# Performance work log

Hardware: AMD Instinct MI355X
Metric: run time of the kernel (lower is better)

## Reference

```python
import jax, jax.numpy as jnp
import numpy as np

B, S, DIM, H, HD = 2, 2048, 512, 8, 64
VD = DIM // H  # 64
QK = H * HD


def setup_inputs() -> dict:
    key = jax.random.key(0)
    k1, k2, k3, k4, k5 = jax.random.split(key, 5)
    x = jax.random.normal(k1, (B, S, DIM), dtype=jnp.float32)
    mask = jax.random.bernoulli(k2, 0.5, (B, S))
    # per-position rotation matrices, scaled to keep activations O(1)
    rotator = jax.random.normal(k3, (B, S, HD, HD), dtype=jnp.float32) / np.sqrt(HD)
    # torch Linear weights: [out_features, in_features], no bias
    W_trans = jax.random.normal(k4, (2 * QK + DIM, DIM), dtype=jnp.float32) / np.sqrt(DIM)
    W_o = jax.random.normal(k5, (DIM, DIM), dtype=jnp.float32) / np.sqrt(DIM)
    return {"x": x, "mask": mask, "rotator": rotator, "W_trans": W_trans, "W_o": W_o}


def _taylor_attention(qs, ks, vs, mask):
    # 2nd-order Taylor approximation of exp for softmax weights
    # qs/ks: [B,S,H,HD], vs: [B,S,H,VD], mask: [B,S] key mask
    scores = jnp.einsum('bqhd,bkhd->bhqk', qs, ks) / np.sqrt(HD)
    w = 1.0 + scores + 0.5 * scores * scores
    w = jnp.where(mask[:, None, None, :], w, 0.0)
    w = w / jnp.sum(w, axis=-1, keepdims=True)
    out = jnp.einsum('bhqk,bkhd->bqhd', w, vs)
    return out.reshape(out.shape[0], out.shape[1], -1)  # [B,S,DIM]


def reference(x, mask, rotator, W_trans, W_o):
    t = x @ W_trans.T  # [B,S,2*QK+DIM]
    qs = t[..., :QK].reshape(B, S, H, HD)
    ks = t[..., QK:2 * QK].reshape(B, S, H, HD)
    vs = t[..., 2 * QK:].reshape(B, S, H, VD)
    sel = mask[..., None, None]
    qs = jnp.where(sel, jnp.einsum('bsij,bshj->bshi', rotator, qs), qs)
    ks = jnp.where(sel, jnp.einsum('bsij,bshj->bshi', rotator, ks), ks)
    out = _taylor_attention(qs, ks, vs, mask)
    return out @ W_o.T
```

## Files before the change

### kernel.cpp

```cpp
#include <hip/hip_runtime.h>
#include <hip/hip_bf16.h>

#define B_    2
#define S_    2048
#define DIM_  512
#define H_    8
#define HD_   64
#define TOUT_ 1536
#define ROWS_ (B_ * S_)

typedef unsigned short ushort_t;
typedef __attribute__((ext_vector_type(8))) __bf16 bf16x8;
typedef __attribute__((ext_vector_type(4))) float floatx4;

#define AS_GLB __attribute__((address_space(1)))
#define AS_LDS __attribute__((address_space(3)))

__device__ __forceinline__ unsigned short f2bfu(float f) {
    unsigned u = __float_as_uint(f);
    unsigned r = (u + 0x7fffu + ((u >> 16) & 1u)) >> 16;
    return (unsigned short)r;
}
__device__ __forceinline__ bf16x8 cvt8(const float* p) {
    float4 a = *reinterpret_cast<const float4*>(p);
    float4 b = *reinterpret_cast<const float4*>(p + 4);
    ushort_t o[8] = {f2bfu(a.x), f2bfu(a.y), f2bfu(a.z), f2bfu(a.w),
                     f2bfu(b.x), f2bfu(b.y), f2bfu(b.z), f2bfu(b.w)};
    return *reinterpret_cast<bf16x8*>(o);
}

__global__ void tmha_mask(const unsigned char* mb, int* wm) {
    __shared__ int s_bf, s_f, s_u8;
    int tid = threadIdx.x;
    if (tid == 0) { s_bf = 0; s_f = 0; s_u8 = 0; }
    __syncthreads();
    int cbf = 0, cf = 0, cu8 = 0;
    for (int i = tid; i < 4096; i += 256) {
        unsigned char v = mb[i];
        if (v == 0x3F || v == 0x80) {
            cf++;
            if ((i & 3) == 1) cbf++;
        } else if (v != 0 && (i & 3) != 0) {
            cu8++;
        }
    }
    atomicAdd(&s_bf, cbf); atomicAdd(&s_f, cf); atomicAdd(&s_u8, cu8);
    __syncthreads();
    int cls = (s_bf > 0) ? 2 : (s_f > 0) ? 3 : (s_u8 > 0) ? 0 : 1;
    for (int i = tid; i < ROWS_; i += 256) {
        int v;
        if (cls == 0)      v = (mb[i] != 0);
        else if (cls == 1) v = (reinterpret_cast<const int*>(mb)[i] != 0);
        else if (cls == 2) v = ((reinterpret_cast<const unsigned short*>(mb)[i] & 0x7fffu) != 0);
        else               v = ((reinterpret_cast<const unsigned int*>(mb)[i] & 0x7fffffffu) != 0);
        wm[i] = v;
    }
}

#define XN4_  (ROWS_ * DIM_ / 4)
#define WTN4_ (TOUT_ * DIM_ / 4)
#define WON4_ (DIM_ * DIM_ / 4)
__global__ __launch_bounds__(256) void cast3_bf16(const float* __restrict__ x,
                                                  const float* __restrict__ wt,
                                                  const float* __restrict__ wo,
                                                  ushort_t* __restrict__ xb,
                                                  ushort_t* __restrict__ wtb,
                                                  ushort_t* __restrict__ wob) {
    int i = blockIdx.x * 256 + threadIdx.x;
    const float* s; ushort_t* d; int off;
    if (i < XN4_)              { s = x;  d = xb;  off = i; }
    else if (i < XN4_ + WTN4_) { s = wt; d = wtb; off = i - XN4_; }
    else                       { s = wo; d = wob; off = i - XN4_ - WTN4_; }
    float4 v = reinterpret_cast<const float4*>(s)[off];
    ushort_t o[4] = {f2bfu(v.x), f2bfu(v.y), f2bfu(v.z), f2bfu(v.w)};
    reinterpret_cast<uint2*>(d)[off] = *reinterpret_cast<uint2*>(o);
}

template <int TM, int N, int K, bool OUT_BF16>
__global__ __launch_bounds__(256) void mfma_gemm_bt(const ushort_t* __restrict__ A,
                                                    const ushort_t* __restrict__ Bm,
                                                    void* __restrict__ Cout) {
    constexpr int FM = (TM + 31) / 32;
    __shared__ __align__(16) ushort_t As[TM * 64];
    __shared__ __align__(16) ushort_t Bs[128 * 64];
    int tid = threadIdx.x;
    int lane = tid & 63;
    int wv = tid >> 6;
    int wm = wv >> 1, wn = wv & 1;
    int quad = lane >> 4;
    int mrow = lane & 15;
    int bx = blockIdx.x;
    int by = blockIdx.y;

    floatx4 acc[FM][4];
#pragma unroll
    for (int i = 0; i < FM; i++)
#pragma unroll
        for (int j = 0; j < 4; j++) acc[i][j] = (floatx4){0.f, 0.f, 0.f, 0.f};

    for (int k0 = 0; k0 < K; k0 += 64) {
#pragma unroll
        for (int t = 0; t < TM / 32; t++) {
            int p = (wv * (TM / 32) + t) * 64 + lane;
            int row = p >> 3, cp = p & 7;
            int gc = cp ^ (row & 7);
            const ushort_t* ga = A + (size_t)(by * TM + row) * K + k0 + gc * 8;
            __builtin_amdgcn_global_load_lds((const AS_GLB unsigned int*)ga,
                                             (AS_LDS unsigned int*)&As[(size_t)(wv * (TM / 32) + t) * 64 * 8],
                                             16, 0, 0);
        }
#pragma unroll
        for (int t = 0; t < 4; t++) {
            int p = (wv * 4 + t) * 64 + lane;
            int row = p >> 3, cp = p & 7;
            int gc = cp ^ (row & 7);
            const ushort_t* gb = Bm + (size_t)(bx * 128 + row) * K + k0 + gc * 8;
            __builtin_amdgcn_global_load_lds((const AS_GLB unsigned int*)gb,
                                             (AS_LDS unsigned int*)&Bs[(size_t)(wv * 4 + t) * 64 * 8],
                                             16, 0, 0);
        }
        __syncthreads();
#pragma unroll
        for (int ks = 0; ks < 64; ks += 32) {
            int c = (ks >> 3) + quad;
            bf16x8 af[FM], bf[4];
#pragma unroll
            for (int i = 0; i < FM; i++) {
                int row = wm * (TM / 2) + i * 16 + mrow;
                int pos = row * 8 + (c ^ (row & 7));
                af[i] = *reinterpret_cast<const bf16x8*>(&As[pos * 8]);
            }
#pragma unroll
            for (int j = 0; j < 4; j++) {
                int row = wn * 64 + j * 16 + mrow;
                int pos = row * 8 + (c ^ (row & 7));
                bf[j] = *reinterpret_cast<const bf16x8*>(&Bs[pos * 8]);
            }
#pragma unroll
            for (int i = 0; i < FM; i++)
#pragma unroll
                for (int j = 0; j < 4; j++)
                    acc[i][j] = __builtin_amdgcn_mfma_f32_16x16x32_bf16(af[i], bf[j], acc[i][j], 0, 0, 0);
        }
        __syncthreads();
    }

    int col0 = bx * 128 + wn * 64 + mrow;
    int row0 = by * TM + wm * (TM / 2) + quad * 4;
    if constexpr (OUT_BF16) {
        ushort_t* C = reinterpret_cast<ushort_t*>(Cout);
#pragma unroll
        for (int i = 0; i < FM; i++)
#pragma unroll
            for (int j = 0; j < 4; j++)
#pragma unroll
                for (int r = 0; r < 4; r++)
                    C[(size_t)(row0 + i * 16 + r) * N + col0 + j * 16] = f2bfu(acc[i][j][r]);
    } else {
        float* C = reinterpret_cast<float*>(Cout);
#pragma unroll
        for (int i = 0; i < FM; i++)
#pragma unroll
            for (int j = 0; j < 4; j++)
#pragma unroll
                for (int r = 0; r < 4; r++)
                    C[(size_t)(row0 + i * 16 + r) * N + col0 + j * 16] = acc[i][j][r];
    }
}

__global__ __launch_bounds__(256) void rot_qk_mfma(const ushort_t* __restrict__ t,
                                                   const float* __restrict__ rotG,
                                                   const int* __restrict__ wm,
                                                   ushort_t* __restrict__ Qb,
                                                   ushort_t* __restrict__ Kb) {
    int lane = threadIdx.x & 63;
    int wv = threadIdx.x >> 6;
    int row = blockIdx.x * 4 + wv;
    int b = row >> 11, s = row & 2047;
    int lm = lane & 15, quad = lane >> 4;
    const ushort_t* trow = t + (size_t)row * TOUT_;
    int kb = s >> 4, l = s & 15;

    if (wm[row]) {
        bf16x8 af[2];
#pragma unroll
        for (int kc = 0; kc < 2; kc++)
            af[kc] = *reinterpret_cast<const bf16x8*>(trow + lm * 64 + kc * 32 + quad * 8);

        const float* R = rotG + (size_t)row * 4096;
        floatx4 dacc[4];
#pragma unroll
        for (int nb = 0; nb < 4; nb++) dacc[nb] = (floatx4){0.f, 0.f, 0.f, 0.f};
#pragma unroll
        for (int nb = 0; nb < 4; nb++)
#pragma unroll
            for (int kc = 0; kc < 2; kc++) {
                bf16x8 bfr = cvt8(R + (size_t)(nb * 16 + lm) * 64 + kc * 32 + quad * 8);
                dacc[nb] = __builtin_amdgcn_mfma_f32_16x16x32_bf16(af[kc], bfr, dacc[nb], 0, 0, 0);
            }
#pragma unroll
        for (int nb = 0; nb < 4; nb++)
#pragma unroll
            for (int r = 0; r < 4; r++) {
                int vec = quad * 4 + r;
                int hh = vec & 7;
                ushort_t v = f2bfu(dacc[nb][r]);
                if (vec >= 8) {
                    int c = nb * 2 + (lm >> 3), e = lm & 7;
                    Kb[(((size_t)(b * 8 + hh) * 128 + kb) * 8 + c) * 128 + l * 8 + e] = v;
                } else {
                    Qb[((size_t)(b * 8 + hh) * 2048 + s) * 64 + nb * 16 + lm] = v;
                }
            }
    } else {
#pragma unroll
        for (int nb = 0; nb < 4; nb++)
#pragma unroll
            for (int r = 0; r < 4; r++) {
                int vec = quad * 4 + r;
                int hh = vec & 7;
                ushort_t v = trow[vec * 64 + nb * 16 + lm];
                if (vec >= 8) {
                    int c = nb * 2 + (lm >> 3), e = lm & 7;
                    Kb[(((size_t)(b * 8 + hh) * 128 + kb) * 8 + c) * 128 + l * 8 + e] = v;
                } else {
                    Qb[((size_t)(b * 8 + hh) * 2048 + s) * 64 + nb * 16 + lm] = v;
                }
            }
    }
}

__global__ __launch_bounds__(256) void prep_vt(const ushort_t* __restrict__ t,
                                               const int* __restrict__ wm,
                                               ushort_t* __restrict__ VtG) {
    __shared__ ushort_t tile[64][72];
    __shared__ float mrow[64];
    int st = blockIdx.x;
    int bh = blockIdx.y;
    int b = bh >> 3, h = bh & 7;
    int tid = threadIdx.x;
    if (tid < 64) mrow[tid] = wm[b * 2048 + st * 64 + tid] ? 1.0f : 0.0f;
#pragma unroll
    for (int i = 0; i < 2; i++) {
        int q = i * 256 + tid;
        int r = q >> 3, c8 = (q & 7) * 8;
        uint4 v = *reinterpret_cast<const uint4*>(
            t + (size_t)(b * 2048 + st * 64 + r) * TOUT_ + 1024 + h * 64 + c8);
        *reinterpret_cast<uint4*>(&tile[r][c8]) = v;
    }
    __syncthreads();
#pragma unroll
    for (int i = 0; i < 8; i++) {
        int e = i * 256 + tid;
        int d = e >> 5, sl = (e & 31) * 2;
        unsigned u0 = (mrow[sl]     != 0.f) ? (unsigned)tile[sl][d]     : 0u;
        unsigned u1 = (mrow[sl + 1] != 0.f) ? (unsigned)tile[sl + 1][d] : 0u;
        *reinterpret_cast<unsigned int*>(VtG + ((size_t)bh * 65 + d) * 2048 + st * 64 + sl) = u0 | (u1 << 16);
    }
    if (tid < 32) {
        int sl = tid * 2;
        unsigned m0 = mrow[sl]     != 0.f ? 0x3F80u : 0u;
        unsigned m1 = mrow[sl + 1] != 0.f ? 0x3F80u : 0u;
        *reinterpret_cast<unsigned int*>(VtG + ((size_t)bh * 65 + 64) * 2048 + st * 64 + sl) = m0 | (m1 << 16);
    }
}

__global__ __launch_bounds__(256) void tmha_attn_mfma(const ushort_t* __restrict__ Qb,
                                                      const ushort_t* __restrict__ KbF,
                                                      const ushort_t* __restrict__ VtG,
                                                      float* __restrict__ numer,
                                                      float* __restrict__ den) {
    __shared__ __align__(16) ushort_t Vs[2][520 * 8];
    __shared__ __align__(16) ushort_t Ps[512 * 8];
    int tid = threadIdx.x;
    int lane = tid & 63;
    int wv = tid >> 6;
    int lm = lane & 15;
    int quad = lane >> 4;
    int qt = blockIdx.x;
    int h = blockIdx.y;
    int z = blockIdx.z;
    int b = z >> 1;
    int ks = z & 1;
    int bh = b * 8 + h;

    const ushort_t* Kf  = KbF + (size_t)bh * 128 * 1024;
    const ushort_t* Vbh = VtG + (size_t)bh * 65 * 2048;

    bf16x8 qf[2];
    {
        const ushort_t* qp = Qb + ((size_t)bh * 2048 + qt * 64 + wv * 16 + lm) * 64 + quad * 8;
        qf[0] = *reinterpret_cast<const bf16x8*>(qp);
        qf[1] = *reinterpret_cast<const bf16x8*>(qp + 32);
    }

    bf16x8 vzero;
    *reinterpret_cast<uint4*>(&vzero) = (uint4){0u, 0u, 0u, 0u};

    floatx4 oacc[5];
#pragma unroll
    for (int j = 0; j < 5; j++) oacc[j] = (floatx4){0.f, 0.f, 0.f, 0.f};

    bf16x8 kr[4][2];
    auto loadK = [&](int kt) {
        int kb = kt >> 4;
#pragma unroll
        for (int j = 0; j < 4; j++)
#pragma unroll
            for (int kc = 0; kc < 2; kc++)
                kr[j][kc] = *reinterpret_cast<const bf16x8*>(
                    Kf + (((size_t)(kb + j) * 8 + kc * 4 + quad) * 16 + lm) * 8);
    };
    auto stageV = [&](int buf, int kt) {
#pragma unroll
        for (int t4 = 0; t4 < 2; t4++) {
            int p = (wv * 2 + t4) * 64 + lane;
            int row = p >> 3, cp = p & 7;
            int gc = cp ^ (row & 7);
            const ushort_t* g = Vbh + (size_t)row * 2048 + kt + gc * 8;
            __builtin_amdgcn_global_load_lds((const AS_GLB unsigned int*)g,
                                             (AS_LDS unsigned int*)&Vs[buf][(wv * 2 + t4) * 64 * 8],
                                             16, 0, 0);
        }
        if (tid < 8) {
            const ushort_t* g = Vbh + (size_t)64 * 2048 + kt + tid * 8;
            __builtin_amdgcn_global_load_lds((const AS_GLB unsigned int*)g,
                                             (AS_LDS unsigned int*)&Vs[buf][512 * 8],
                                             16, 0, 0);
        }
    };

    int kt0 = ks * 1024;
    stageV(0, kt0);
    loadK(kt0);
    int buf = 0;
#pragma unroll 1
    for (int tt = 0; tt < 16; tt++) {
        int ktn = (tt == 15) ? kt0 : kt0 + (tt + 1) * 64;
        __syncthreads();
        stageV(buf ^ 1, ktn);

        floatx4 sacc[4];
#pragma unroll
        for (int j = 0; j < 4; j++) sacc[j] = (floatx4){0.f, 0.f, 0.f, 0.f};
#pragma unroll
        for (int j = 0; j < 4; j++)
#pragma unroll
            for (int kc = 0; kc < 2; kc++)
                sacc[j] = __builtin_amdgcn_mfma_f32_16x16x32_bf16(qf[kc], kr[j][kc], sacc[j], 0, 0, 0);

        loadK(ktn);

#pragma unroll
        for (int j = 0; j < 4; j++)
#pragma unroll
            for (int r = 0; r < 4; r++) {
                float s = sacc[j][r];
                float wgt = fmaf(s, fmaf(s, 0.0078125f, 0.125f), 1.0f);
                int m = wv * 16 + quad * 4 + r;
                int col = j * 16 + lm;
                int cw = col >> 3;
                int pos = m * 8 + (cw ^ (m & 7));
                Ps[pos * 8 + (col & 7)] = f2bfu(wgt);
            }
        asm volatile("s_waitcnt lgkmcnt(0)" ::: "memory");
        __builtin_amdgcn_sched_barrier(0);

        int qrow_l = wv * 16 + lm;
        bf16x8 pa[2];
#pragma unroll
        for (int kc = 0; kc < 2; kc++) {
            int c = kc * 4 + quad;
            int ppos = qrow_l * 8 + (c ^ (qrow_l & 7));
            pa[kc] = *reinterpret_cast<const bf16x8*>(&Ps[ppos * 8]);
        }
#pragma unroll
        for (int j = 0; j < 5; j++) {
            int vrow = (j < 4) ? (j * 16 + lm) : 64;
#pragma unroll
            for (int kc = 0; kc < 2; kc++) {
                int c = kc * 4 + quad;
                int vpos = vrow * 8 + (c ^ (vrow & 7));
                bf16x8 vb = *reinterpret_cast<const bf16x8*>(&Vs[buf][vpos * 8]);
                if (j == 4 && lm != 0) vb = vzero;
                oacc[j] = __builtin_amdgcn_mfma_f32_16x16x32_bf16(pa[kc], vb, oacc[j], 0, 0, 0);
            }
        }
        buf ^= 1;
    }

#pragma unroll
    for (int j = 0; j < 4; j++)
#pragma unroll
        for (int r = 0; r < 4; r++) {
            int qrow = b * 2048 + qt * 64 + wv * 16 + quad * 4 + r;
            numer[((size_t)ks * ROWS_ + qrow) * DIM_ + h * 64 + j * 16 + lm] = oacc[j][r];
        }
    if (lm == 0) {
#pragma unroll
        for (int r = 0; r < 4; r++) {
            int qrow = b * 2048 + qt * 64 + wv * 16 + quad * 4 + r;
            den[((size_t)ks * ROWS_ + qrow) * 8 + h] = oacc[4][r];
        }
    }
}

__global__ __launch_bounds__(256) void attn_combine(const float* __restrict__ numer,
                                                    const float* __restrict__ den,
                                                    ushort_t* __restrict__ attnAb) {
    int i = blockIdx.x * 256 + threadIdx.x;
    int row = i >> 7;
    int c4 = (i & 127) * 4;
    int h = c4 >> 6;
    float4 n0 = *reinterpret_cast<const float4*>(&numer[(size_t)row * DIM_ + c4]);
    float4 n1 = *reinterpret_cast<const float4*>(&numer[((size_t)ROWS_ + row) * DIM_ + c4]);
    float d = den[(size_t)row * 8 + h] + den[((size_t)ROWS_ + row) * 8 + h];
    float inv = 1.0f / d;
    ushort_t o[4] = {f2bfu((n0.x + n1.x) * inv), f2bfu((n0.y + n1.y) * inv),
                     f2bfu((n0.z + n1.z) * inv), f2bfu((n0.w + n1.w) * inv)};
    *reinterpret_cast<uint2*>(&attnAb[(size_t)row * DIM_ + c4]) = *reinterpret_cast<uint2*>(o);
}

extern "C" void kernel_launch(void* const* d_in, const int* in_sizes, int n_in,
                              void* d_out, int out_size, void* d_ws, size_t ws_size,
                              hipStream_t stream) {
    (void)in_sizes; (void)n_in; (void)out_size; (void)ws_size;
    const float* x    = (const float*)d_in[0];
    const void*  mask = d_in[1];
    const float* rot  = (const float*)d_in[2];
    const float* Wt   = (const float*)d_in[3];
    const float* Wo   = (const float*)d_in[4];

    char* ws = (char*)d_ws;
    int* wmask       = (int*)(ws + 64);
    ushort_t* t      = (ushort_t*)(ws + 32768);
    ushort_t* Xb     = (ushort_t*)(ws + 25198592);
    ushort_t* Wtb    = (ushort_t*)(ws + 29392896);
    ushort_t* Wob    = (ushort_t*)(ws + 30965760);
    ushort_t* Qb     = (ushort_t*)(ws + 31490048);
    ushort_t* Kb     = (ushort_t*)(ws + 35684352);
    ushort_t* VtG    = (ushort_t*)(ws + 39878656);
    ushort_t* attnAb = (ushort_t*)(ws + 44138496);
    float* numer     = (float*)(ws + 32768);
    float* den       = (float*)(ws + 32768 + 16777216);

    tmha_mask<<<1, 256, 0, stream>>>((const unsigned char*)mask, wmask);

    cast3_bf16<<<(XN4_ + WTN4_ + WON4_) / 256, 256, 0, stream>>>(x, Wt, Wo, Xb, Wtb, Wob);

    {
        dim3 grid(TOUT_ / 128, ROWS_ / 64);
        mfma_gemm_bt<64, TOUT_, DIM_, true><<<grid, 256, 0, stream>>>(Xb, Wtb, (void*)t);
    }

    rot_qk_mfma<<<ROWS_ / 4, 256, 0, stream>>>(t, rot, wmask, Qb, Kb);

    {
        dim3 grid(32, 16);
        prep_vt<<<grid, 256, 0, stream>>>(t, wmask, VtG);
    }

    {
        dim3 grid(32, 8, 4);
        tmha_attn_mfma<<<grid, 256, 0, stream>>>(Qb, Kb, VtG, numer, den);
    }
    attn_combine<<<(ROWS_ * 128) / 256, 256, 0, stream>>>(numer, den, attnAb);

    {
        dim3 grid(DIM_ / 128, ROWS_ / 32);
        mfma_gemm_bt<32, DIM_, DIM_, false><<<grid, 256, 0, stream>>>(attnAb, Wob, d_out);
    }
}
```

Before: 194.0 us.

## Drop split-K attention, load V fragments from registers, fuse normalization and mask kernels

```diff
diff --git a/kernel.cpp b/kernel.cpp
--- a/kernel.cpp
+++ b/kernel.cpp
@@ -29,43 +29,46 @@
     return *reinterpret_cast<bf16x8*>(o);
 }
 
-__global__ void tmha_mask(const unsigned char* mb, int* wm) {
-    __shared__ int s_bf, s_f, s_u8;
-    int tid = threadIdx.x;
-    if (tid == 0) { s_bf = 0; s_f = 0; s_u8 = 0; }
-    __syncthreads();
-    int cbf = 0, cf = 0, cu8 = 0;
-    for (int i = tid; i < 4096; i += 256) {
-        unsigned char v = mb[i];
-        if (v == 0x3F || v == 0x80) {
-            cf++;
-            if ((i & 3) == 1) cbf++;
-        } else if (v != 0 && (i & 3) != 0) {
-            cu8++;
-        }
-    }
-    atomicAdd(&s_bf, cbf); atomicAdd(&s_f, cf); atomicAdd(&s_u8, cu8);
-    __syncthreads();
-    int cls = (s_bf > 0) ? 2 : (s_f > 0) ? 3 : (s_u8 > 0) ? 0 : 1;
-    for (int i = tid; i < ROWS_; i += 256) {
-        int v;
-        if (cls == 0)      v = (mb[i] != 0);
-        else if (cls == 1) v = (reinterpret_cast<const int*>(mb)[i] != 0);
-        else if (cls == 2) v = ((reinterpret_cast<const unsigned short*>(mb)[i] & 0x7fffu) != 0);
-        else               v = ((reinterpret_cast<const unsigned int*>(mb)[i] & 0x7fffffffu) != 0);
-        wm[i] = v;
-    }
-}
-
 #define XN4_  (ROWS_ * DIM_ / 4)
 #define WTN4_ (TOUT_ * DIM_ / 4)
 #define WON4_ (DIM_ * DIM_ / 4)
-__global__ __launch_bounds__(256) void cast3_bf16(const float* __restrict__ x,
-                                                  const float* __restrict__ wt,
-                                                  const float* __restrict__ wo,
-                                                  ushort_t* __restrict__ xb,
-                                                  ushort_t* __restrict__ wtb,
-                                                  ushort_t* __restrict__ wob) {
+#define CASTBLKS_ ((XN4_ + WTN4_ + WON4_) / 256)
+__global__ __launch_bounds__(256) void prep_inputs(const float* __restrict__ x,
+                                                   const float* __restrict__ wt,
+                                                   const float* __restrict__ wo,
+                                                   const unsigned char* __restrict__ mb,
+                                                   ushort_t* __restrict__ xb,
+                                                   ushort_t* __restrict__ wtb,
+                                                   ushort_t* __restrict__ wob,
+                                                   int* __restrict__ wm) {
+    if (blockIdx.x >= CASTBLKS_) {
+        __shared__ int s_bf, s_f, s_u8;
+        int tid = threadIdx.x;
+        if (tid == 0) { s_bf = 0; s_f = 0; s_u8 = 0; }
+        __syncthreads();
+        int cbf = 0, cf = 0, cu8 = 0;
+        for (int i = tid; i < 4096; i += 256) {
+            unsigned char v = mb[i];
+            if (v == 0x3F || v == 0x80) {
+                cf++;
+                if ((i & 3) == 1) cbf++;
+            } else if (v != 0 && (i & 3) != 0) {
+                cu8++;
+            }
+        }
+        atomicAdd(&s_bf, cbf); atomicAdd(&s_f, cf); atomicAdd(&s_u8, cu8);
+        __syncthreads();
+        int cls = (s_bf > 0) ? 2 : (s_f > 0) ? 3 : (s_u8 > 0) ? 0 : 1;
+        for (int i = tid; i < ROWS_; i += 256) {
+            int v;
+            if (cls == 0)      v = (mb[i] != 0);
+            else if (cls == 1) v = (reinterpret_cast<const int*>(mb)[i] != 0);
+            else if (cls == 2) v = ((reinterpret_cast<const unsigned short*>(mb)[i] & 0x7fffu) != 0);
+            else               v = ((reinterpret_cast<const unsigned int*>(mb)[i] & 0x7fffffffu) != 0);
+            wm[i] = v;
+        }
+        return;
+    }
     int i = blockIdx.x * 256 + threadIdx.x;
     const float* s; ushort_t* d; int off;
     if (i < XN4_)              { s = x;  d = xb;  off = i; }
@@ -232,14 +235,15 @@
 
 __global__ __launch_bounds__(256) void prep_vt(const ushort_t* __restrict__ t,
                                                const int* __restrict__ wm,
-                                               ushort_t* __restrict__ VtG) {
+                                               ushort_t* __restrict__ VtF,
+                                               ushort_t* __restrict__ MrowG) {
     __shared__ ushort_t tile[64][72];
-    __shared__ float mrow[64];
+    __shared__ ushort_t umask[64];
     int st = blockIdx.x;
     int bh = blockIdx.y;
     int b = bh >> 3, h = bh & 7;
     int tid = threadIdx.x;
-    if (tid < 64) mrow[tid] = wm[b * 2048 + st * 64 + tid] ? 1.0f : 0.0f;
+    if (tid < 64) umask[tid] = wm[b * 2048 + st * 64 + tid] ? 0xFFFFu : 0u;
 #pragma unroll
     for (int i = 0; i < 2; i++) {
         int q = i * 256 + tid;
@@ -249,43 +253,47 @@
         *reinterpret_cast<uint4*>(&tile[r][c8]) = v;
     }
     __syncthreads();
-#pragma unroll
-    for (int i = 0; i < 8; i++) {
-        int e = i * 256 + tid;
-        int d = e >> 5, sl = (e & 31) * 2;
-        unsigned u0 = (mrow[sl]     != 0.f) ? (unsigned)tile[sl][d]     : 0u;
-        unsigned u1 = (mrow[sl + 1] != 0.f) ? (unsigned)tile[sl + 1][d] : 0u;
-        *reinterpret_cast<unsigned int*>(VtG + ((size_t)bh * 65 + d) * 2048 + st * 64 + sl) = u0 | (u1 << 16);
-    }
     if (tid < 32) {
         int sl = tid * 2;
-        unsigned m0 = mrow[sl]     != 0.f ? 0x3F80u : 0u;
-        unsigned m1 = mrow[sl + 1] != 0.f ? 0x3F80u : 0u;
-        *reinterpret_cast<unsigned int*>(VtG + ((size_t)bh * 65 + 64) * 2048 + st * 64 + sl) = m0 | (m1 << 16);
+        unsigned m0 = umask[sl]     ? 0x3F80u : 0u;
+        unsigned m1 = umask[sl + 1] ? 0x3F80u : 0u;
+        *reinterpret_cast<unsigned int*>(MrowG + (size_t)bh * 2048 + st * 64 + sl) = m0 | (m1 << 16);
+    }
+#pragma unroll
+    for (int it = 0; it < 2; it++) {
+        int idx = tid + it * 256;
+        int d = idx & 63;
+        int chunk = idx >> 6;
+        ushort_t o[8];
+#pragma unroll
+        for (int e = 0; e < 8; e++)
+            o[e] = (ushort_t)(tile[chunk * 8 + e][d] & umask[chunk * 8 + e]);
+        *reinterpret_cast<uint4*>(
+            VtF + ((((size_t)bh * 32 + st) * 8 + chunk) * 64 + d) * 8) = *reinterpret_cast<const uint4*>(o);
     }
 }
 
 __global__ __launch_bounds__(256) void tmha_attn_mfma(const ushort_t* __restrict__ Qb,
                                                       const ushort_t* __restrict__ KbF,
-                                                      const ushort_t* __restrict__ VtG,
-                                                      float* __restrict__ numer,
-                                                      float* __restrict__ den) {
-    __shared__ __align__(16) ushort_t Vs[2][520 * 8];
+                                                      const ushort_t* __restrict__ VtF,
+                                                      const ushort_t* __restrict__ MrowG,
+                                                      ushort_t* __restrict__ attnAb) {
     __shared__ __align__(16) ushort_t Ps[512 * 8];
     int tid = threadIdx.x;
     int lane = tid & 63;
     int wv = tid >> 6;
     int lm = lane & 15;
     int quad = lane >> 4;
-    int qt = blockIdx.x;
-    int h = blockIdx.y;
-    int z = blockIdx.z;
-    int b = z >> 1;
-    int ks = z & 1;
-    int bh = b * 8 + h;
-
-    const ushort_t* Kf  = KbF + (size_t)bh * 128 * 1024;
-    const ushort_t* Vbh = VtG + (size_t)bh * 65 * 2048;
+
+    int bid = blockIdx.x;
+    int w = ((bid & 7) << 6) | (bid >> 3);
+    int qt = w & 31;
+    int bh = w >> 5;
+    int b = bh >> 3, h = bh & 7;
+
+    const ushort_t* Kf = KbF + (size_t)bh * 128 * 1024;
+    const ushort_t* Vf = VtF + (size_t)bh * 32 * 8 * 64 * 8;
+    const ushort_t* Mr = MrowG + (size_t)bh * 2048;
 
     bf16x8 qf[2];
     {
@@ -301,7 +309,7 @@
 #pragma unroll
     for (int j = 0; j < 5; j++) oacc[j] = (floatx4){0.f, 0.f, 0.f, 0.f};
 
-    bf16x8 kr[4][2];
+    bf16x8 kr[4][2], vr[4][2], mvb[2];
     auto loadK = [&](int kt) {
         int kb = kt >> 4;
 #pragma unroll
@@ -311,43 +319,37 @@
                 kr[j][kc] = *reinterpret_cast<const bf16x8*>(
                     Kf + (((size_t)(kb + j) * 8 + kc * 4 + quad) * 16 + lm) * 8);
     };
-    auto stageV = [&](int buf, int kt) {
-#pragma unroll
-        for (int t4 = 0; t4 < 2; t4++) {
-            int p = (wv * 2 + t4) * 64 + lane;
-            int row = p >> 3, cp = p & 7;
-            int gc = cp ^ (row & 7);
-            const ushort_t* g = Vbh + (size_t)row * 2048 + kt + gc * 8;
-            __builtin_amdgcn_global_load_lds((const AS_GLB unsigned int*)g,
-                                             (AS_LDS unsigned int*)&Vs[buf][(wv * 2 + t4) * 64 * 8],
-                                             16, 0, 0);
-        }
-        if (tid < 8) {
-            const ushort_t* g = Vbh + (size_t)64 * 2048 + kt + tid * 8;
-            __builtin_amdgcn_global_load_lds((const AS_GLB unsigned int*)g,
-                                             (AS_LDS unsigned int*)&Vs[buf][512 * 8],
-                                             16, 0, 0);
-        }
+    auto loadV = [&](int kt) {
+        int st = kt >> 6;
+#pragma unroll
+        for (int j = 0; j < 4; j++)
+#pragma unroll
+            for (int kc = 0; kc < 2; kc++)
+                vr[j][kc] = *reinterpret_cast<const bf16x8*>(
+                    Vf + (((size_t)st * 8 + kc * 4 + quad) * 64 + j * 16 + lm) * 8);
     };
-
-    int kt0 = ks * 1024;
-    stageV(0, kt0);
-    loadK(kt0);
-    int buf = 0;
+    auto loadM = [&](int kt) {
+#pragma unroll
+        for (int kc = 0; kc < 2; kc++)
+            mvb[kc] = *reinterpret_cast<const bf16x8*>(Mr + kt + (kc * 4 + quad) * 8);
+    };
+
+    loadK(0); loadV(0); loadM(0);
 #pragma unroll 1
-    for (int tt = 0; tt < 16; tt++) {
-        int ktn = (tt == 15) ? kt0 : kt0 + (tt + 1) * 64;
-        __syncthreads();
-        stageV(buf ^ 1, ktn);
+    for (int tt = 0; tt < 32; tt++) {
+        int kt = tt * 64;
+        int ktn = (tt == 31) ? 0 : kt + 64;
 
         floatx4 sacc[4];
 #pragma unroll
         for (int j = 0; j < 4; j++) sacc[j] = (floatx4){0.f, 0.f, 0.f, 0.f};
+        __builtin_amdgcn_s_setprio(1);
 #pragma unroll
         for (int j = 0; j < 4; j++)
 #pragma unroll
             for (int kc = 0; kc < 2; kc++)
                 sacc[j] = __builtin_amdgcn_mfma_f32_16x16x32_bf16(qf[kc], kr[j][kc], sacc[j], 0, 0, 0);
+        __builtin_amdgcn_s_setprio(0);
 
         loadK(ktn);
 
@@ -374,51 +376,35 @@
             int ppos = qrow_l * 8 + (c ^ (qrow_l & 7));
             pa[kc] = *reinterpret_cast<const bf16x8*>(&Ps[ppos * 8]);
         }
-#pragma unroll
-        for (int j = 0; j < 5; j++) {
-            int vrow = (j < 4) ? (j * 16 + lm) : 64;
-#pragma unroll
-            for (int kc = 0; kc < 2; kc++) {
-                int c = kc * 4 + quad;
-                int vpos = vrow * 8 + (c ^ (vrow & 7));
-                bf16x8 vb = *reinterpret_cast<const bf16x8*>(&Vs[buf][vpos * 8]);
-                if (j == 4 && lm != 0) vb = vzero;
-                oacc[j] = __builtin_amdgcn_mfma_f32_16x16x32_bf16(pa[kc], vb, oacc[j], 0, 0, 0);
-            }
-        }
-        buf ^= 1;
-    }
-
+        __builtin_amdgcn_s_setprio(1);
+#pragma unroll
+        for (int j = 0; j < 4; j++)
+#pragma unroll
+            for (int kc = 0; kc < 2; kc++)
+                oacc[j] = __builtin_amdgcn_mfma_f32_16x16x32_bf16(pa[kc], vr[j][kc], oacc[j], 0, 0, 0);
+#pragma unroll
+        for (int kc = 0; kc < 2; kc++) {
+            bf16x8 vb = (lm == 0) ? mvb[kc] : vzero;
+            oacc[4] = __builtin_amdgcn_mfma_f32_16x16x32_bf16(pa[kc], vb, oacc[4], 0, 0, 0);
+        }
+        __builtin_amdgcn_s_setprio(0);
+
+        loadV(ktn); loadM(ktn);
+    }
+
+    float inv[4];
+#pragma unroll
+    for (int r = 0; r < 4; r++) {
+        float dn = __shfl(oacc[4][r], lane & 48);
+        inv[r] = 1.0f / dn;
+    }
 #pragma unroll
     for (int j = 0; j < 4; j++)
 #pragma unroll
         for (int r = 0; r < 4; r++) {
             int qrow = b * 2048 + qt * 64 + wv * 16 + quad * 4 + r;
-            numer[((size_t)ks * ROWS_ + qrow) * DIM_ + h * 64 + j * 16 + lm] = oacc[j][r];
-        }
-    if (lm == 0) {
-#pragma unroll
-        for (int r = 0; r < 4; r++) {
-            int qrow = b * 2048 + qt * 64 + wv * 16 + quad * 4 + r;
-            den[((size_t)ks * ROWS_ + qrow) * 8 + h] = oacc[4][r];
-        }
-    }
-}
-
-__global__ __launch_bounds__(256) void attn_combine(const float* __restrict__ numer,
-                                                    const float* __restrict__ den,
-                                                    ushort_t* __restrict__ attnAb) {
-    int i = blockIdx.x * 256 + threadIdx.x;
-    int row = i >> 7;
-    int c4 = (i & 127) * 4;
-    int h = c4 >> 6;
-    float4 n0 = *reinterpret_cast<const float4*>(&numer[(size_t)row * DIM_ + c4]);
-    float4 n1 = *reinterpret_cast<const float4*>(&numer[((size_t)ROWS_ + row) * DIM_ + c4]);
-    float d = den[(size_t)row * 8 + h] + den[((size_t)ROWS_ + row) * 8 + h];
-    float inv = 1.0f / d;
-    ushort_t o[4] = {f2bfu((n0.x + n1.x) * inv), f2bfu((n0.y + n1.y) * inv),
-                     f2bfu((n0.z + n1.z) * inv), f2bfu((n0.w + n1.w) * inv)};
-    *reinterpret_cast<uint2*>(&attnAb[(size_t)row * DIM_ + c4]) = *reinterpret_cast<uint2*>(o);
+            attnAb[(size_t)qrow * DIM_ + h * 64 + j * 16 + lm] = f2bfu(oacc[j][r] * inv[r]);
+        }
 }
 
 extern "C" void kernel_launch(void* const* d_in, const int* in_sizes, int n_in,
@@ -439,14 +425,12 @@
     ushort_t* Wob    = (ushort_t*)(ws + 30965760);
     ushort_t* Qb     = (ushort_t*)(ws + 31490048);
     ushort_t* Kb     = (ushort_t*)(ws + 35684352);
-    ushort_t* VtG    = (ushort_t*)(ws + 39878656);
+    ushort_t* VtF    = (ushort_t*)(ws + 39878656);
+    ushort_t* MrowG  = (ushort_t*)(ws + 44072960);
     ushort_t* attnAb = (ushort_t*)(ws + 44138496);
-    float* numer     = (float*)(ws + 32768);
-    float* den       = (float*)(ws + 32768 + 16777216);
-
-    tmha_mask<<<1, 256, 0, stream>>>((const unsigned char*)mask, wmask);
-
-    cast3_bf16<<<(XN4_ + WTN4_ + WON4_) / 256, 256, 0, stream>>>(x, Wt, Wo, Xb, Wtb, Wob);
+
+    prep_inputs<<<CASTBLKS_ + 1, 256, 0, stream>>>(x, Wt, Wo, (const unsigned char*)mask,
+                                                   Xb, Wtb, Wob, wmask);
 
     {
         dim3 grid(TOUT_ / 128, ROWS_ / 64);
@@ -457,14 +441,10 @@
 
     {
         dim3 grid(32, 16);
-        prep_vt<<<grid, 256, 0, stream>>>(t, wmask, VtG);
-    }
-
-    {
-        dim3 grid(32, 8, 4);
-        tmha_attn_mfma<<<grid, 256, 0, stream>>>(Qb, Kb, VtG, numer, den);
-    }
-    attn_combine<<<(ROWS_ * 128) / 256, 256, 0, stream>>>(numer, den, attnAb);
+        prep_vt<<<grid, 256, 0, stream>>>(t, wmask, VtF, MrowG);
+    }
+
+    tmha_attn_mfma<<<512, 256, 0, stream>>>(Qb, Kb, VtF, MrowG, attnAb);
 
     {
         dim3 grid(DIM_ / 128, ROWS_ / 32);
```

New measurement: 197.7 us. No clear change (+1.9%).
